# Optimization experiments

Measured on AMD Instinct MI355X. Metric: run time of the kernel, lower is better.

## Reference

```python
import jax, jax.numpy as jnp
import numpy as np


def setup_inputs() -> dict:
    key = jax.random.key(0)
    ks = jax.random.split(key, 5)
    B, P_LEN, D = 16, 1024, 512
    scale = 0.02
    return {
        "P": jax.random.normal(ks[0], (B, P_LEN, D), dtype=jnp.float32),
        "w_atten": jax.random.normal(ks[1], (3 * D,), dtype=jnp.float32) * scale,
        "w1": jax.random.normal(ks[2], (2 * D, D), dtype=jnp.float32) * scale,
        "w2": jax.random.normal(ks[3], (2 * D, D), dtype=jnp.float32) * scale,
        "w3": jax.random.normal(ks[4], (2 * D, D), dtype=jnp.float32) * scale,
        "b1": jnp.zeros((D,), dtype=jnp.float32),
        "b2": jnp.zeros((D,), dtype=jnp.float32),
        "b3": jnp.zeros((D,), dtype=jnp.float32),
    }


def reference(P, w_atten, w1, w2, w3, b1, b2, b3):
    # P: (b, p, d). Original builds a (b, p, 3d, p) concat tensor; the score
    # A[b,i,j] = wa . P_i + wb . P_j + wc . (P_i * P_j) factorizes exactly:
    d = P.shape[-1]
    wa, wb, wc = w_atten[:d], w_atten[d:2 * d], w_atten[2 * d:]
    si = P @ wa                                   # (b, p)  contribution of row token i
    sj = P @ wb                                   # (b, p)  contribution of col token j
    A = si[:, :, None] + sj[:, None, :] + jnp.einsum("bid,bjd->bij", P * wc, P)
    SA = jax.nn.softmax(A, axis=2)                # softmax over j
    attn_res = jnp.einsum("bij,bjd->bid", SA, P)  # (b, p, d)
    # Fuse gate (DecayingDropout is identity at inference)
    Pc = jnp.concatenate([P, attn_res], axis=2)   # (b, p, 2d)
    z = jnp.tanh(Pc @ w1 + b1)
    r = jax.nn.sigmoid(Pc @ w2 + b2)
    f = jax.nn.sigmoid(Pc @ w3 + b3)
    return r * P + f * z
```

## Files before the change

### kernel.cpp

```cpp
#include <hip/hip_runtime.h>
#include <stdint.h>

#define S_LEN 1024
#define DDIM  512
#define NBATCH 16

typedef __attribute__((ext_vector_type(8))) short bf16x8;
typedef __attribute__((ext_vector_type(4))) float f32x4;

__device__ __forceinline__ unsigned short f2bf(float x) {
  union { float f; uint32_t u; } v; v.f = x;
  return (unsigned short)((v.u + 0x7fffu + ((v.u >> 16) & 1u)) >> 16);
}
__device__ __forceinline__ float bf2f(unsigned short h) {
  union { float f; uint32_t u; } v; v.u = ((uint32_t)h) << 16;
  return v.f;
}

__device__ __forceinline__ void gload16(const void* g, void* l) {
  __builtin_amdgcn_global_load_lds(
      (const __attribute__((address_space(1))) void*)g,
      (__attribute__((address_space(3))) void*)l, 16, 0, 0);
}

__global__ __launch_bounds__(256) void prep_rows(
    const float* __restrict__ P, const float* __restrict__ w_atten,
    unsigned short* __restrict__ Pbf, unsigned short* __restrict__ Qbf,
    float* __restrict__ sj) {
  int wave = threadIdx.x >> 6, lane = threadIdx.x & 63;
  int row = blockIdx.x * 4 + wave;
  const float* prow = P + (size_t)row * DDIM;
  float s = 0.f;
#pragma unroll
  for (int h = 0; h < 2; ++h) {
    int d = h * 256 + lane * 4;
    float4 p  = *(const float4*)(prow + d);
    float4 wb = *(const float4*)(w_atten + DDIM + d);
    float4 wc = *(const float4*)(w_atten + 2 * DDIM + d);
    s += p.x * wb.x + p.y * wb.y + p.z * wb.z + p.w * wb.w;
    ushort4 pb, qb;
    pb.x = f2bf(p.x); pb.y = f2bf(p.y); pb.z = f2bf(p.z); pb.w = f2bf(p.w);
    qb.x = f2bf(p.x * wc.x); qb.y = f2bf(p.y * wc.y);
    qb.z = f2bf(p.z * wc.z); qb.w = f2bf(p.w * wc.w);
    *(ushort4*)(Pbf + (size_t)row * DDIM + d) = pb;
    *(ushort4*)(Qbf + (size_t)row * DDIM + d) = qb;
  }
#pragma unroll
  for (int o = 32; o; o >>= 1) s += __shfl_xor(s, o);
  if (lane == 0) sj[row] = s;
}

__global__ __launch_bounds__(256) void transpose_f2b(
    const float* __restrict__ in, unsigned short* __restrict__ out,
    int R, int C, long inStride, long outStride) {
  __shared__ unsigned short T[64][65];
  in  += (size_t)blockIdx.z * inStride;
  out += (size_t)blockIdx.z * outStride;
  int c0 = blockIdx.x * 64, r0 = blockIdx.y * 64;
  int tx = threadIdx.x & 63, ty = threadIdx.x >> 6;
#pragma unroll
  for (int rr = 0; rr < 16; ++rr) {
    int rl = ty * 16 + rr;
    T[rl][tx] = f2bf(in[(size_t)(r0 + rl) * C + c0 + tx]);
  }
  __syncthreads();
#pragma unroll
  for (int rr = 0; rr < 16; ++rr) {
    int cl = ty * 16 + rr;
    out[(size_t)(c0 + cl) * R + r0 + tx] = T[tx][cl];
  }
}

template<int EPI>
__global__ __launch_bounds__(256) void gemm_nt(
    const unsigned short* __restrict__ A,
    const unsigned short* __restrict__ A2,
    const unsigned short* __restrict__ Bt,
    unsigned short* __restrict__ C,
    const float* __restrict__ bias,
    const float* __restrict__ bias2,
    const float* __restrict__ bias3,
    int N, int K, int lda, int Ksplit,
    long sAb, long sBb, long sCb, long sBiasb) {
  __shared__ __align__(16) unsigned short lA[2][128 * 32];
  __shared__ __align__(16) unsigned short lB[2][128 * 32];
  const int t = threadIdx.x;
  const int lane = t & 63;
  const int wave = t >> 6;
  const int z = blockIdx.z;
  A  += (size_t)z * sAb;
  if (A2) A2 += (size_t)z * sAb;
  Bt += (size_t)z * sBb;
  C  += (size_t)z * sCb;
  if (bias) bias += (size_t)z * sBiasb;
  const int bm = blockIdx.y * 128, bn = blockIdx.x * 128;

  f32x4 acc[4][4];
#pragma unroll
  for (int m = 0; m < 4; ++m)
#pragma unroll
    for (int n = 0; n < 4; ++n) acc[m][n] = {0.f, 0.f, 0.f, 0.f};

  const int wr = wave >> 1, wc = wave & 1;
  const int frow = lane & 15;
  const int fk = (lane >> 4) * 8;
  const int srow = t >> 2;
  const int skc = (t & 3) * 8;
  const int lbase = (t & 192) * 8;

  auto stage = [&](int buf, int k0) {
    const unsigned short* Asrc = A;
    int ka = k0;
    if (A2 != nullptr && k0 >= Ksplit) { Asrc = A2; ka = k0 - Ksplit; }
#pragma unroll
    for (int r2 = 0; r2 < 2; ++r2)
      gload16(Asrc + (size_t)(bm + r2 * 64 + srow) * lda + ka + skc,
              lA[buf] + r2 * 2048 + lbase);
#pragma unroll
    for (int r2 = 0; r2 < 2; ++r2)
      gload16(Bt + (size_t)(bn + r2 * 64 + srow) * K + k0 + skc,
              lB[buf] + r2 * 2048 + lbase);
  };

  stage(0, 0);
  __syncthreads();
  int cur = 0;
  for (int k0 = 0; k0 < K; k0 += 32) {
    if (k0 + 32 < K) stage(cur ^ 1, k0 + 32);
    bf16x8 af[4], bfr[4];
#pragma unroll
    for (int m = 0; m < 4; ++m)
      af[m] = *(const bf16x8*)(lA[cur] + (wr * 64 + m * 16 + frow) * 32 + fk);
#pragma unroll
    for (int n = 0; n < 4; ++n)
      bfr[n] = *(const bf16x8*)(lB[cur] + (wc * 64 + n * 16 + frow) * 32 + fk);
#pragma unroll
    for (int m = 0; m < 4; ++m)
#pragma unroll
      for (int n = 0; n < 4; ++n)
        acc[m][n] = __builtin_amdgcn_mfma_f32_16x16x32_bf16(af[m], bfr[n], acc[m][n], 0, 0, 0);
    __syncthreads();
    cur ^= 1;
  }

  const int seg = bn >> 9;
  const float* bp = bias;
  if (EPI == 4) bp = (seg == 0) ? bias : ((seg == 1) ? bias2 : bias3);
#pragma unroll
  for (int m = 0; m < 4; ++m) {
    int row0 = bm + wr * 64 + m * 16 + (lane >> 4) * 4;
#pragma unroll
    for (int n = 0; n < 4; ++n) {
      int col = bn + wc * 64 + n * 16 + (lane & 15);
      float bc = (EPI >= 1) ? bp[(EPI == 4) ? (col & 511) : col] : 0.f;
#pragma unroll
      for (int i = 0; i < 4; ++i) {
        float v = acc[m][n][i];
        if (EPI == 1) v += bc;
        if (EPI == 4) {
          v += bc;
          v = (seg == 0) ? tanhf(v) : 1.f / (1.f + __expf(-v));
        }
        C[(size_t)(row0 + i) * N + col] = f2bf(v);
      }
    }
  }
}

__global__ __launch_bounds__(256) void softmax_rows(unsigned short* __restrict__ Sb) {
  __shared__ float red[8];
  unsigned short* p = Sb + (size_t)blockIdx.x * S_LEN;
  int t = threadIdx.x, wave = t >> 6, lane = t & 63;
  ushort4 u = *(ushort4*)(p + t * 4);
  float v0 = bf2f(u.x), v1 = bf2f(u.y), v2 = bf2f(u.z), v3 = bf2f(u.w);
  float mx = fmaxf(fmaxf(v0, v1), fmaxf(v2, v3));
#pragma unroll
  for (int o = 32; o; o >>= 1) mx = fmaxf(mx, __shfl_xor(mx, o));
  if (lane == 0) red[wave] = mx;
  __syncthreads();
  mx = fmaxf(fmaxf(red[0], red[1]), fmaxf(red[2], red[3]));
  float e0 = __expf(v0 - mx), e1 = __expf(v1 - mx);
  float e2 = __expf(v2 - mx), e3 = __expf(v3 - mx);
  float ss = e0 + e1 + e2 + e3;
#pragma unroll
  for (int o = 32; o; o >>= 1) ss += __shfl_xor(ss, o);
  if (lane == 0) red[4 + wave] = ss;
  __syncthreads();
  float inv = 1.f / (red[4] + red[5] + red[6] + red[7]);
  u.x = f2bf(e0 * inv); u.y = f2bf(e1 * inv);
  u.z = f2bf(e2 * inv); u.w = f2bf(e3 * inv);
  *(ushort4*)(p + t * 4) = u;
}

__global__ __launch_bounds__(256) void final_out(
    const float* __restrict__ P, const unsigned short* __restrict__ Cm,
    float* __restrict__ out) {
  size_t i = ((size_t)blockIdx.x * 256 + threadIdx.x) * 4;
  size_t row = i >> 9;
  int col = (int)(i & 511);
  const unsigned short* base = Cm + row * 1536 + col;
  ushort4 z4 = *(const ushort4*)(base);
  ushort4 r4 = *(const ushort4*)(base + 512);
  ushort4 f4 = *(const ushort4*)(base + 1024);
  float4 p = *(const float4*)(P + i);
  float4 o;
  o.x = bf2f(r4.x) * p.x + bf2f(f4.x) * bf2f(z4.x);
  o.y = bf2f(r4.y) * p.y + bf2f(f4.y) * bf2f(z4.y);
  o.z = bf2f(r4.z) * p.z + bf2f(f4.z) * bf2f(z4.z);
  o.w = bf2f(r4.w) * p.w + bf2f(f4.w) * bf2f(z4.w);
  *(float4*)(out + i) = o;
}

extern "C" void kernel_launch(void* const* d_in, const int* in_sizes, int n_in,
                              void* d_out, int out_size, void* d_ws, size_t ws_size,
                              hipStream_t stream) {
  const float* P  = (const float*)d_in[0];
  const float* wa = (const float*)d_in[1];
  const float* w1 = (const float*)d_in[2];
  const float* w2 = (const float*)d_in[3];
  const float* w3 = (const float*)d_in[4];
  const float* b1 = (const float*)d_in[5];
  const float* b2 = (const float*)d_in[6];
  const float* b3 = (const float*)d_in[7];
  float* out = (float*)d_out;
  char* ws = (char*)d_ws;
  const size_t MB = 1024 * 1024;

  unsigned short* Pbf  = (unsigned short*)(ws + 0);
  unsigned short* PT   = (unsigned short*)(ws + 16 * MB);
  unsigned short* Qbf  = (unsigned short*)(ws + 32 * MB);
  unsigned short* Sbuf = (unsigned short*)(ws + 48 * MB);
  unsigned short* attn = (unsigned short*)(ws + 80 * MB);
  unsigned short* Wt   = (unsigned short*)(ws + 96 * MB);
  float*          sj   = (float*)(ws + 99 * MB);
  unsigned short* Cmlp = (unsigned short*)(ws + 16 * MB);

  const long SD = (long)S_LEN * DDIM;
  const long SS = (long)S_LEN * S_LEN;

  prep_rows<<<4096, 256, 0, stream>>>(P, wa, Pbf, Qbf, sj);
  transpose_f2b<<<dim3(8, 16, NBATCH), 256, 0, stream>>>(P, PT, S_LEN, DDIM, SD, SD);
  transpose_f2b<<<dim3(8, 16, 1), 256, 0, stream>>>(w1, Wt,          1024, 512, 0, 0);
  transpose_f2b<<<dim3(8, 16, 1), 256, 0, stream>>>(w2, Wt + SD,     1024, 512, 0, 0);
  transpose_f2b<<<dim3(8, 16, 1), 256, 0, stream>>>(w3, Wt + 2 * SD, 1024, 512, 0, 0);

  gemm_nt<1><<<dim3(8, 8, NBATCH), 256, 0, stream>>>(
      Qbf, nullptr, Pbf, Sbuf, sj, nullptr, nullptr,
      1024, 512, 512, 0, SD, SD, SS, S_LEN);
  softmax_rows<<<16384, 256, 0, stream>>>(Sbuf);
  gemm_nt<0><<<dim3(4, 8, NBATCH), 256, 0, stream>>>(
      Sbuf, nullptr, PT, attn, nullptr, nullptr, nullptr,
      512, 1024, 1024, 0, SS, SD, SD, 0);
  gemm_nt<4><<<dim3(12, 128, 1), 256, 0, stream>>>(
      Pbf, attn, Wt, Cmlp, b1, b2, b3,
      1536, 1024, 512, 512, 0, 0, 0, 0);

  final_out<<<8192, 256, 0, stream>>>(P, Cmlp, out);
}
```

Before: 213.3 us.

## Replace GEMM with 256x256-tile 8-wave pipelined kernel using swizzled LDS

Replaces the 128x128 double-buffered GEMM with a 256x256 tile, 512-thread kernel that uses a 64-wide K step, four-phase interleaving of global-to-LDS staging with MFMA quadrants, XOR-swizzled LDS layout, and s_setprio around MFMA bursts. The aim is more data reuse per tile, fewer LDS bank conflicts, and overlap of memory loads with matrix math. In exchange it uses 128KB of LDS and more accumulator registers per thread, and launches far fewer blocks (e.g. 256 blocks for the score GEMM, 128 for the attention GEMM), which may underfill the GPU's compute units.

Measured after the change: 218.4 us. 2.4% more time.

```diff
diff --git a/kernel.cpp b/kernel.cpp
--- a/kernel.cpp
+++ b/kernel.cpp
@@ -7,6 +7,7 @@
 
 typedef __attribute__((ext_vector_type(8))) short bf16x8;
 typedef __attribute__((ext_vector_type(4))) float f32x4;
+typedef unsigned short ushort_t;
 
 __device__ __forceinline__ unsigned short f2bf(float x) {
   union { float f; uint32_t u; } v; v.f = x;
@@ -71,87 +72,120 @@
   }
 }
 
+#define STAGE_A(buf, h, kt_) do { int k0_ = (kt_) * 64; const ushort_t* s_ = A;   \
+    if (A2 != nullptr && k0_ >= Ksplit) { s_ = A2; k0_ -= Ksplit; }               \
+    ushort_t* d_ = &lds[((buf) * 2 + (h)) * 8192 + w * 1024];                     \
+    const ushort_t* g_ = s_ + (size_t)(bm + (h) * 128 + srow) * lda + k0_ + scol; \
+    gload16(g_, d_); gload16(g_ + 32, d_ + 512); } while (0)
+
+#define STAGE_B(buf, h, kt_) do { int k0_ = (kt_) * 64;                           \
+    ushort_t* d_ = &lds[32768 + ((buf) * 2 + (h)) * 8192 + w * 1024];             \
+    const ushort_t* g_ = Bt + (size_t)(bn + (h) * 128 + srow) * K + k0_ + scol;   \
+    gload16(g_, d_); gload16(g_ + 32, d_ + 512); } while (0)
+
+#define READ_A(mh) do { const char* ab_ = (const char*)&lds[(cur * 2 + wr) * 8192]; \
+    _Pragma("unroll") for (int m_ = 0; m_ < 4; ++m_)                                \
+    _Pragma("unroll") for (int ks_ = 0; ks_ < 2; ++ks_)                             \
+      af[m_][ks_] = *(const bf16x8*)(ab_ + ((((mh) * 4 + m_) * 2 + ks_) << 10)      \
+                                     + rl * 64 + swzc); } while (0)
+
+#define READ_B(nh) do { const char* bb_ = (const char*)&lds[32768 + (cur * 2 + (wc >> 1)) * 8192]; \
+    _Pragma("unroll") for (int n_ = 0; n_ < 2; ++n_)                                \
+    _Pragma("unroll") for (int ks_ = 0; ks_ < 2; ++ks_)                             \
+      bfr[(nh) * 2 + n_][ks_] = *(const bf16x8*)(bb_ +                              \
+          ((((wc & 1) * 4 + (nh) * 2 + n_) * 2 + ks_) << 10) + rl * 64 + swzc); } while (0)
+
+#define MFMA_Q(mh, nh) do {                                                       \
+    __builtin_amdgcn_s_setprio(1);                                                \
+    _Pragma("unroll") for (int m_ = 0; m_ < 4; ++m_)                              \
+    _Pragma("unroll") for (int n_ = 0; n_ < 2; ++n_) {                            \
+      f32x4 a_ = acc[(mh) * 4 + m_][(nh) * 2 + n_];                               \
+      a_ = __builtin_amdgcn_mfma_f32_16x16x32_bf16(af[m_][0], bfr[(nh)*2+n_][0], a_, 0, 0, 0); \
+      a_ = __builtin_amdgcn_mfma_f32_16x16x32_bf16(af[m_][1], bfr[(nh)*2+n_][1], a_, 0, 0, 0); \
+      acc[(mh) * 4 + m_][(nh) * 2 + n_] = a_; }                                   \
+    __builtin_amdgcn_s_setprio(0); } while (0)
+
+#define PHASE_SYNC() do { __builtin_amdgcn_s_barrier();                           \
+    asm volatile("s_waitcnt lgkmcnt(0)" ::: "memory");                            \
+    __builtin_amdgcn_sched_barrier(0); } while (0)
+
 template<int EPI>
-__global__ __launch_bounds__(256) void gemm_nt(
-    const unsigned short* __restrict__ A,
-    const unsigned short* __restrict__ A2,
-    const unsigned short* __restrict__ Bt,
-    unsigned short* __restrict__ C,
+__global__ __launch_bounds__(512, 2) void gemm8(
+    const ushort_t* __restrict__ A,
+    const ushort_t* __restrict__ A2,
+    const ushort_t* __restrict__ Bt,
+    ushort_t* __restrict__ C,
     const float* __restrict__ bias,
     const float* __restrict__ bias2,
     const float* __restrict__ bias3,
     int N, int K, int lda, int Ksplit,
     long sAb, long sBb, long sCb, long sBiasb) {
-  __shared__ __align__(16) unsigned short lA[2][128 * 32];
-  __shared__ __align__(16) unsigned short lB[2][128 * 32];
-  const int t = threadIdx.x;
-  const int lane = t & 63;
-  const int wave = t >> 6;
+  __shared__ __align__(16) ushort_t lds[65536];
+  const int t = threadIdx.x, lane = t & 63, w = t >> 6;
+  const int wr = w >> 2, wc = w & 3;
   const int z = blockIdx.z;
-  A  += (size_t)z * sAb;
+  A += (size_t)z * sAb;
   if (A2) A2 += (size_t)z * sAb;
   Bt += (size_t)z * sBb;
-  C  += (size_t)z * sCb;
+  C += (size_t)z * sCb;
   if (bias) bias += (size_t)z * sBiasb;
-  const int bm = blockIdx.y * 128, bn = blockIdx.x * 128;
-
-  f32x4 acc[4][4];
-#pragma unroll
-  for (int m = 0; m < 4; ++m)
+  const int bm = blockIdx.y * 256, bn = blockIdx.x * 256;
+  const int NT = K >> 6;
+
+  const int rl = lane & 15;
+  const int swzc = ((lane >> 4) << 4) ^ ((lane & 8) << 2);
+  const int srow = w * 16 + (lane >> 2);
+  const int scol = ((lane & 3) * 8) ^ ((lane & 32) >> 1);
+
+  f32x4 acc[8][4];
+#pragma unroll
+  for (int m = 0; m < 8; ++m)
 #pragma unroll
     for (int n = 0; n < 4; ++n) acc[m][n] = {0.f, 0.f, 0.f, 0.f};
-
-  const int wr = wave >> 1, wc = wave & 1;
-  const int frow = lane & 15;
-  const int fk = (lane >> 4) * 8;
-  const int srow = t >> 2;
-  const int skc = (t & 3) * 8;
-  const int lbase = (t & 192) * 8;
-
-  auto stage = [&](int buf, int k0) {
-    const unsigned short* Asrc = A;
-    int ka = k0;
-    if (A2 != nullptr && k0 >= Ksplit) { Asrc = A2; ka = k0 - Ksplit; }
-#pragma unroll
-    for (int r2 = 0; r2 < 2; ++r2)
-      gload16(Asrc + (size_t)(bm + r2 * 64 + srow) * lda + ka + skc,
-              lA[buf] + r2 * 2048 + lbase);
-#pragma unroll
-    for (int r2 = 0; r2 < 2; ++r2)
-      gload16(Bt + (size_t)(bn + r2 * 64 + srow) * K + k0 + skc,
-              lB[buf] + r2 * 2048 + lbase);
-  };
-
-  stage(0, 0);
-  __syncthreads();
-  int cur = 0;
-  for (int k0 = 0; k0 < K; k0 += 32) {
-    if (k0 + 32 < K) stage(cur ^ 1, k0 + 32);
-    bf16x8 af[4], bfr[4];
-#pragma unroll
-    for (int m = 0; m < 4; ++m)
-      af[m] = *(const bf16x8*)(lA[cur] + (wr * 64 + m * 16 + frow) * 32 + fk);
-#pragma unroll
-    for (int n = 0; n < 4; ++n)
-      bfr[n] = *(const bf16x8*)(lB[cur] + (wc * 64 + n * 16 + frow) * 32 + fk);
-#pragma unroll
-    for (int m = 0; m < 4; ++m)
-#pragma unroll
-      for (int n = 0; n < 4; ++n)
-        acc[m][n] = __builtin_amdgcn_mfma_f32_16x16x32_bf16(af[m], bfr[n], acc[m][n], 0, 0, 0);
-    __syncthreads();
-    cur ^= 1;
+  bf16x8 af[4][2], bfr[4][2];
+
+  STAGE_A(0, 0, 0); STAGE_A(0, 1, 0);
+  STAGE_B(0, 0, 0); STAGE_B(0, 1, 0);
+  STAGE_B(1, 0, 1); STAGE_B(1, 1, 1);
+  asm volatile("s_waitcnt vmcnt(4)" ::: "memory");
+  __builtin_amdgcn_s_barrier();
+
+  for (int kt = 0; kt < NT; ++kt) {
+    const int cur = kt & 1, nxt = cur ^ 1;
+    READ_A(0); READ_B(0);
+    if (kt + 1 < NT) STAGE_A(nxt, 0, kt + 1);
+    PHASE_SYNC();
+    MFMA_Q(0, 0);
+    __builtin_amdgcn_s_barrier();
+    READ_B(1);
+    if (kt + 1 < NT) STAGE_A(nxt, 1, kt + 1);
+    PHASE_SYNC();
+    MFMA_Q(0, 1);
+    __builtin_amdgcn_s_barrier();
+    READ_A(1);
+    if (kt + 2 < NT) STAGE_B(cur, 0, kt + 2);
+    PHASE_SYNC();
+    MFMA_Q(1, 0);
+    __builtin_amdgcn_s_barrier();
+    if (kt + 2 < NT) STAGE_B(cur, 1, kt + 2);
+    PHASE_SYNC();
+    MFMA_Q(1, 1);
+    if (kt + 1 < NT) {
+      if (kt + 2 < NT) asm volatile("s_waitcnt vmcnt(4)" ::: "memory");
+      else             asm volatile("s_waitcnt vmcnt(0)" ::: "memory");
+    }
+    __builtin_amdgcn_s_barrier();
   }
 
   const int seg = bn >> 9;
   const float* bp = bias;
   if (EPI == 4) bp = (seg == 0) ? bias : ((seg == 1) ? bias2 : bias3);
 #pragma unroll
-  for (int m = 0; m < 4; ++m) {
-    int row0 = bm + wr * 64 + m * 16 + (lane >> 4) * 4;
+  for (int m = 0; m < 8; ++m) {
+    int row0 = bm + wr * 128 + m * 16 + (lane >> 4) * 4;
 #pragma unroll
     for (int n = 0; n < 4; ++n) {
-      int col = bn + wc * 64 + n * 16 + (lane & 15);
+      int col = bn + wc * 64 + n * 16 + rl;
       float bc = (EPI >= 1) ? bp[(EPI == 4) ? (col & 511) : col] : 0.f;
 #pragma unroll
       for (int i = 0; i < 4; ++i) {
@@ -244,14 +278,14 @@
   transpose_f2b<<<dim3(8, 16, 1), 256, 0, stream>>>(w2, Wt + SD,     1024, 512, 0, 0);
   transpose_f2b<<<dim3(8, 16, 1), 256, 0, stream>>>(w3, Wt + 2 * SD, 1024, 512, 0, 0);
 
-  gemm_nt<1><<<dim3(8, 8, NBATCH), 256, 0, stream>>>(
+  gemm8<1><<<dim3(4, 4, NBATCH), 512, 0, stream>>>(
       Qbf, nullptr, Pbf, Sbuf, sj, nullptr, nullptr,
       1024, 512, 512, 0, SD, SD, SS, S_LEN);
   softmax_rows<<<16384, 256, 0, stream>>>(Sbuf);
-  gemm_nt<0><<<dim3(4, 8, NBATCH), 256, 0, stream>>>(
+  gemm8<0><<<dim3(2, 4, NBATCH), 512, 0, stream>>>(
       Sbuf, nullptr, PT, attn, nullptr, nullptr, nullptr,
       512, 1024, 1024, 0, SS, SD, SD, 0);
-  gemm_nt<4><<<dim3(12, 128, 1), 256, 0, stream>>>(
+  gemm8<4><<<dim3(6, 64, 1), 512, 0, stream>>>(
       Pbf, attn, Wt, Cmlp, b1, b2, b3,
       1536, 1024, 512, 512, 0, 0, 0, 0);
 
```

## Triple-buffer GEMM LDS pipeline with XCD-aware block remapping

Applied to the files above, without the earlier changes.

Replaces the double-buffered GEMM main loop with a three-stage LDS ring buffer, so loads run two tiles ahead. Waits on outstanding loads use explicit vmcnt counts, with one raw s_barrier per iteration and raised wave priority around the MFMA block. Blocks are also remapped so consecutive hardware block IDs, which are spread round-robin across the 8 XCDs, land on contiguous tiles, aiming for better L2 reuse. This costs more LDS per block (48KB instead of 32KB), which may reduce occupancy, and the hand-written waitcnt logic is fragile.

New measurement: 219.5 us. +2.9%, slower.

```diff
diff --git a/kernel.cpp b/kernel.cpp
--- a/kernel.cpp
+++ b/kernel.cpp
@@ -7,6 +7,7 @@
 
 typedef __attribute__((ext_vector_type(8))) short bf16x8;
 typedef __attribute__((ext_vector_type(4))) float f32x4;
+typedef unsigned short ushort_t;
 
 __device__ __forceinline__ unsigned short f2bf(float x) {
   union { float f; uint32_t u; } v; v.f = x;
@@ -72,28 +73,35 @@
 }
 
 template<int EPI>
-__global__ __launch_bounds__(256) void gemm_nt(
-    const unsigned short* __restrict__ A,
-    const unsigned short* __restrict__ A2,
-    const unsigned short* __restrict__ Bt,
-    unsigned short* __restrict__ C,
+__global__ __launch_bounds__(256) void gemm_tb(
+    const ushort_t* __restrict__ A,
+    const ushort_t* __restrict__ A2,
+    const ushort_t* __restrict__ Bt,
+    ushort_t* __restrict__ C,
     const float* __restrict__ bias,
     const float* __restrict__ bias2,
     const float* __restrict__ bias3,
     int N, int K, int lda, int Ksplit,
     long sAb, long sBb, long sCb, long sBiasb) {
-  __shared__ __align__(16) unsigned short lA[2][128 * 32];
-  __shared__ __align__(16) unsigned short lB[2][128 * 32];
-  const int t = threadIdx.x;
-  const int lane = t & 63;
-  const int wave = t >> 6;
-  const int z = blockIdx.z;
-  A  += (size_t)z * sAb;
+  __shared__ __align__(16) ushort_t lA[3][4096];
+  __shared__ __align__(16) ushort_t lB[3][4096];
+  const int t = threadIdx.x, lane = t & 63, wave = t >> 6;
+
+  const int gx = gridDim.x, gy = gridDim.y;
+  int hblk = blockIdx.x + gx * (blockIdx.y + gy * blockIdx.z);
+  int cpx = (gx * gy * (int)gridDim.z) >> 3;
+  int wk = (hblk & 7) * cpx + (hblk >> 3);
+  const int by = wk % gy; int rem = wk / gy;
+  const int bx = rem % gx;
+  const int z  = rem / gx;
+
+  A += (size_t)z * sAb;
   if (A2) A2 += (size_t)z * sAb;
   Bt += (size_t)z * sBb;
-  C  += (size_t)z * sCb;
+  C += (size_t)z * sCb;
   if (bias) bias += (size_t)z * sBiasb;
-  const int bm = blockIdx.y * 128, bn = blockIdx.x * 128;
+  const int bm = by * 128, bn = bx * 128;
+  const int NT = K >> 5;
 
   f32x4 acc[4][4];
 #pragma unroll
@@ -108,39 +116,58 @@
   const int skc = (t & 3) * 8;
   const int lbase = (t & 192) * 8;
 
-  auto stage = [&](int buf, int k0) {
-    const unsigned short* Asrc = A;
+  auto stageT = [&](ushort_t* dA, ushort_t* dB, int kt) {
+    int k0 = kt << 5;
+    const ushort_t* Asrc = A;
     int ka = k0;
     if (A2 != nullptr && k0 >= Ksplit) { Asrc = A2; ka = k0 - Ksplit; }
 #pragma unroll
     for (int r2 = 0; r2 < 2; ++r2)
       gload16(Asrc + (size_t)(bm + r2 * 64 + srow) * lda + ka + skc,
-              lA[buf] + r2 * 2048 + lbase);
+              dA + r2 * 2048 + lbase);
 #pragma unroll
     for (int r2 = 0; r2 < 2; ++r2)
       gload16(Bt + (size_t)(bn + r2 * 64 + srow) * K + k0 + skc,
-              lB[buf] + r2 * 2048 + lbase);
+              dB + r2 * 2048 + lbase);
   };
 
-  stage(0, 0);
-  __syncthreads();
-  int cur = 0;
-  for (int k0 = 0; k0 < K; k0 += 32) {
-    if (k0 + 32 < K) stage(cur ^ 1, k0 + 32);
+  ushort_t *Ard = lA[0], *Aw1 = lA[1], *Aw2 = lA[2];
+  ushort_t *Brd = lB[0], *Bw1 = lB[1], *Bw2 = lB[2];
+
+  stageT(Ard, Brd, 0);
+  stageT(Aw1, Bw1, 1);
+  asm volatile("s_waitcnt vmcnt(4)" ::: "memory");
+  __builtin_amdgcn_sched_barrier(0);
+  __builtin_amdgcn_s_barrier();
+  __builtin_amdgcn_sched_barrier(0);
+
+  for (int kt = 0; kt < NT; ++kt) {
+    if (kt + 2 < NT) stageT(Aw2, Bw2, kt + 2);
     bf16x8 af[4], bfr[4];
 #pragma unroll
     for (int m = 0; m < 4; ++m)
-      af[m] = *(const bf16x8*)(lA[cur] + (wr * 64 + m * 16 + frow) * 32 + fk);
+      af[m] = *(const bf16x8*)(Ard + (wr * 64 + m * 16 + frow) * 32 + fk);
 #pragma unroll
     for (int n = 0; n < 4; ++n)
-      bfr[n] = *(const bf16x8*)(lB[cur] + (wc * 64 + n * 16 + frow) * 32 + fk);
+      bfr[n] = *(const bf16x8*)(Brd + (wc * 64 + n * 16 + frow) * 32 + fk);
+    asm volatile("s_waitcnt lgkmcnt(0)" ::: "memory");
+    __builtin_amdgcn_sched_barrier(0);
+    __builtin_amdgcn_s_setprio(1);
 #pragma unroll
     for (int m = 0; m < 4; ++m)
 #pragma unroll
       for (int n = 0; n < 4; ++n)
         acc[m][n] = __builtin_amdgcn_mfma_f32_16x16x32_bf16(af[m], bfr[n], acc[m][n], 0, 0, 0);
-    __syncthreads();
-    cur ^= 1;
+    __builtin_amdgcn_s_setprio(0);
+    if (kt + 1 < NT) {
+      if (kt + 2 < NT) asm volatile("s_waitcnt vmcnt(4)" ::: "memory");
+      else             asm volatile("s_waitcnt vmcnt(0)" ::: "memory");
+      __builtin_amdgcn_sched_barrier(0);
+      __builtin_amdgcn_s_barrier();
+      __builtin_amdgcn_sched_barrier(0);
+    }
+    ushort_t* ta = Ard; Ard = Aw1; Aw1 = Aw2; Aw2 = ta;
+    ushort_t* tb = Brd; Brd = Bw1; Bw1 = Bw2; Bw2 = tb;
   }
 
   const int seg = bn >> 9;
@@ -151,7 +178,7 @@
     int row0 = bm + wr * 64 + m * 16 + (lane >> 4) * 4;
 #pragma unroll
     for (int n = 0; n < 4; ++n) {
-      int col = bn + wc * 64 + n * 16 + (lane & 15);
+      int col = bn + wc * 64 + n * 16 + frow;
       float bc = (EPI >= 1) ? bp[(EPI == 4) ? (col & 511) : col] : 0.f;
 #pragma unroll
       for (int i = 0; i < 4; ++i) {
@@ -244,14 +271,14 @@
   transpose_f2b<<<dim3(8, 16, 1), 256, 0, stream>>>(w2, Wt + SD,     1024, 512, 0, 0);
   transpose_f2b<<<dim3(8, 16, 1), 256, 0, stream>>>(w3, Wt + 2 * SD, 1024, 512, 0, 0);
 
-  gemm_nt<1><<<dim3(8, 8, NBATCH), 256, 0, stream>>>(
+  gemm_tb<1><<<dim3(8, 8, NBATCH), 256, 0, stream>>>(
       Qbf, nullptr, Pbf, Sbuf, sj, nullptr, nullptr,
       1024, 512, 512, 0, SD, SD, SS, S_LEN);
   softmax_rows<<<16384, 256, 0, stream>>>(Sbuf);
-  gemm_nt<0><<<dim3(4, 8, NBATCH), 256, 0, stream>>>(
+  gemm_tb<0><<<dim3(4, 8, NBATCH), 256, 0, stream>>>(
       Sbuf, nullptr, PT, attn, nullptr, nullptr, nullptr,
       512, 1024, 1024, 0, SS, SD, SD, 0);
-  gemm_nt<4><<<dim3(12, 128, 1), 256, 0, stream>>>(
+  gemm_tb<4><<<dim3(12, 128, 1), 256, 0, stream>>>(
       Pbf, attn, Wt, Cmlp, b1, b2, b3,
       1536, 1024, 512, 512, 0, 0, 0, 0);
 
```
